# Performance work log

Hardware: AMD Instinct MI355X
Metric: run time of the kernel (lower is better)

## Reference

```python
import jax, jax.numpy as jnp
import numpy as np

B, S, D, H = 4, 2048, 1024, 16
DK = D // H


def setup_inputs() -> dict:
    key = jax.random.key(0)
    ks = jax.random.split(key, 12)
    std = 1.0 / np.sqrt(D)
    return {
        "query": jax.random.normal(ks[0], (B, S, D), jnp.float32),
        "key": jax.random.normal(ks[1], (B, S, D), jnp.float32),
        "value": jax.random.normal(ks[2], (B, S, D), jnp.float32),
        "fc_w": jax.random.normal(ks[3], (D, D), jnp.float32),
        "Wq": jax.random.normal(ks[4], (D, D), jnp.float32) * std,
        "bq": jax.random.normal(ks[5], (D,), jnp.float32) * 0.01,
        "Wk": jax.random.normal(ks[6], (D, D), jnp.float32) * std,
        "bk": jax.random.normal(ks[7], (D,), jnp.float32) * 0.01,
        "Wv": jax.random.normal(ks[8], (D, D), jnp.float32) * std,
        "bv": jax.random.normal(ks[9], (D,), jnp.float32) * 0.01,
        "Wo": jax.random.normal(ks[10], (D, D), jnp.float32) * std,
        "bo": jax.random.normal(ks[11], (D,), jnp.float32) * 0.01,
    }


def reference(query, key, value, fc_w, Wq, bq, Wk, bk, Wv, bv, Wo, bo):
    b = query.shape[0]
    # meta-modulated (scaling) query projection: x @ (fc_w * base_w) + b
    q = jnp.matmul(query, fc_w * Wq) + bq
    k = jnp.matmul(key, Wk) + bk
    v = jnp.matmul(value, Wv) + bv
    # [B, S, D] -> [B, H, S, DK]
    q = q.reshape(b, -1, H, DK).transpose(0, 2, 1, 3)
    k = k.reshape(b, -1, H, DK).transpose(0, 2, 1, 3)
    v = v.reshape(b, -1, H, DK).transpose(0, 2, 1, 3)
    scores = jnp.einsum("bhqd,bhkd->bhqk", q, k) / jnp.sqrt(jnp.float32(DK))
    attn = jax.nn.softmax(scores, axis=-1)  # dropout identity at eval
    x = jnp.einsum("bhqk,bhkd->bhqd", attn, v)
    x = x.transpose(0, 2, 1, 3).reshape(b, -1, H * DK)
    return jnp.matmul(x, Wo) + bo
```

## Files before the change

### kernel.cpp

```cpp
#include <hip/hip_runtime.h>
#include <hip/hip_bf16.h>
#include <stdint.h>

#define BB 4
#define SS 2048
#define DD 1024
#define HH 16
#define DKK 64
#define MT (BB*SS)
#define KK DD

typedef __attribute__((ext_vector_type(8))) short bf16x8;
typedef __attribute__((ext_vector_type(4))) float f32x4;
typedef __attribute__((ext_vector_type(8))) unsigned short u16x8;

__device__ __forceinline__ unsigned short f2bf(float f){
  union { float f; unsigned u; } x; x.f = f;
  unsigned r = x.u + 0x7fffu + ((x.u >> 16) & 1u);
  return (unsigned short)(r >> 16);
}

__device__ __forceinline__ short bfc(float x){
  return (short)__builtin_bit_cast(unsigned short, (__bf16)x);
}

__device__ __forceinline__ float ex2(float x){
#if __has_builtin(__builtin_amdgcn_exp2f)
  return __builtin_amdgcn_exp2f(x);
#else
  return exp2f(x);
#endif
}

__device__ __forceinline__ float fm3(float a, float b, float c){
  return fmaxf(fmaxf(a, b), c);
}

__device__ __forceinline__ void gll16(const void* g, void* l){
  __builtin_amdgcn_global_load_lds(
      (const __attribute__((address_space(1))) void*)g,
      (__attribute__((address_space(3))) void*)l, 16, 0, 0);
}

__global__ __launch_bounds__(256) void cvt_bf16(const float* __restrict__ in,
                                                unsigned short* __restrict__ out){
  int i = blockIdx.x * 256 + threadIdx.x;
  const f32x4* p = (const f32x4*)in;
  f32x4 a = p[2*i], b = p[2*i+1];
  u16x8 o;
  #pragma unroll
  for (int j=0;j<4;j++){ o[j] = f2bf(a[j]); o[4+j] = f2bf(b[j]); }
  ((u16x8*)out)[i] = o;
}

__global__ __launch_bounds__(256) void prep_weights(
    const float* __restrict__ fc, const float* __restrict__ Wq,
    const float* __restrict__ Wk, const float* __restrict__ Wv,
    const float* __restrict__ Wo,
    unsigned short* __restrict__ Wqt, unsigned short* __restrict__ Wkt,
    unsigned short* __restrict__ Wvt, unsigned short* __restrict__ Wot){
  __shared__ float tile[32][33];
  int which = blockIdx.y;
  const float* src = which==0?Wq: which==1?Wk: which==2?Wv:Wo;
  unsigned short* dst = which==0?Wqt: which==1?Wkt: which==2?Wvt:Wot;
  int k0 = (blockIdx.x & 31)*32, n0 = (blockIdx.x >> 5)*32;
  int tid = threadIdx.x;
  #pragma unroll
  for (int i=0;i<4;i++){
    int e = tid + i*256; int r = e>>5, c = e&31;
    float v = src[(size_t)(k0+r)*DD + n0 + c];
    if (which==0) v *= fc[(size_t)(k0+r)*DD + n0 + c];
    tile[r][c] = v;
  }
  __syncthreads();
  #pragma unroll
  for (int i=0;i<4;i++){
    int e = tid + i*256; int r = e>>5, c = e&31;
    dst[(size_t)(n0+r)*DD + k0 + c] = f2bf(tile[c][r]);
  }
}

template<int EPI>
__global__ __launch_bounds__(256) void gemm_bt(
    const unsigned short* __restrict__ A,
    const unsigned short* __restrict__ Bt,
    const float* __restrict__ bias,
    float scale,
    void* __restrict__ Cout){
  __shared__ __align__(16) unsigned short Asb[2][128*32];
  __shared__ __align__(16) unsigned short Bsb[2][128*32];
  const int tid = threadIdx.x;
  const int lane = tid & 63, wid = tid >> 6;
  const int sidx = blockIdx.x;
  const int xcd = sidx & 7, jj = sidx >> 3;
  const int by = xcd*8 + (jj>>3), bx = jj & 7;
  const int m0 = by * 128, n0 = bx * 128;
  const int wm = wid >> 1, wn = wid & 1;
  const int g = lane >> 4, lr = lane & 15;

  f32x4 acc[4][4];
  #pragma unroll
  for (int i=0;i<4;i++)
    #pragma unroll
    for (int j=0;j<4;j++) acc[i][j] = (f32x4){0.f,0.f,0.f,0.f};

  const char* gaBase = (const char*)(A  + (size_t)m0 * KK);
  const char* gbBase = (const char*)(Bt + (size_t)n0 * KK);

  auto stage = [&](int buf, int kt){
    #pragma unroll
    for (int is=0; is<2; ++is){
      int t = is*4096 + wid*1024 + lane*16;
      int row = t >> 6, col = t & 63;
      gll16(gaBase + (size_t)row*(KK*2) + (size_t)kt*64 + col,
            (char*)&Asb[buf][0] + is*4096 + wid*1024);
      gll16(gbBase + (size_t)row*(KK*2) + (size_t)kt*64 + col,
            (char*)&Bsb[buf][0] + is*4096 + wid*1024);
    }
  };

  stage(0, 0);
  __syncthreads();
  int cur = 0;
  for (int kt = 0; kt < KK/32; ++kt){
    if (kt + 1 < KK/32) stage(cur^1, kt+1);
    bf16x8 af[4], bfr[4];
    #pragma unroll
    for (int f=0; f<4; ++f){
      int ar = wm*64 + f*16 + lr;
      af[f]  = *(const bf16x8*)&Asb[cur][ar*32 + g*8];
      int br = wn*64 + f*16 + lr;
      bfr[f] = *(const bf16x8*)&Bsb[cur][br*32 + g*8];
    }
    #pragma unroll
    for (int i=0;i<4;i++)
      #pragma unroll
      for (int j=0;j<4;j++)
        acc[i][j] = __builtin_amdgcn_mfma_f32_16x16x32_bf16(af[i], bfr[j], acc[i][j], 0, 0, 0);
    __syncthreads();
    cur ^= 1;
  }

  #pragma unroll
  for (int j=0;j<4;j++){
    int n = n0 + wn*64 + j*16 + lr;
    float bv = bias[n];
    #pragma unroll
    for (int i=0;i<4;i++){
      int mbase = m0 + wm*64 + i*16 + g*4;
      #pragma unroll
      for (int r=0;r<4;r++){
        int m = mbase + r;
        float v = (acc[i][j][r] + bv) * scale;
        if (EPI == 0){
          int b = m >> 11, s = m & (SS-1);
          int h = n >> 6, dk = n & 63;
          ((unsigned short*)Cout)[(((size_t)(b*HH + h))*SS + s)*DKK + dk] = f2bf(v);
        } else {
          ((float*)Cout)[(size_t)m*DD + n] = v;
        }
      }
    }
  }
}

__global__ __launch_bounds__(256) void transpose_v(const unsigned short* __restrict__ V,
                                                   unsigned short* __restrict__ Vt){
  __shared__ unsigned short t[64][72];
  int bh = blockIdx.y; int s0 = blockIdx.x*64;
  const unsigned short* src = V + ((size_t)bh*SS + s0)*DKK;
  int tid = threadIdx.x;
  #pragma unroll
  for (int i=0;i<2;i++){
    int e = (tid + i*256)*8; int r = e>>6, c = e&63;
    int rp = (r & 35) | ((r & 12) << 1) | ((r & 16) >> 2);
    u16x8 v = *(const u16x8*)(src + (size_t)r*DKK + c);
    #pragma unroll
    for (int j=0;j<8;j++) t[c+j][rp] = v[j];
  }
  __syncthreads();
  unsigned short* dst = Vt + ((size_t)bh*DKK)*SS + s0;
  #pragma unroll
  for (int i=0;i<2;i++){
    int e = (tid + i*256)*8; int d = e>>6, c = e&63;
    u16x8 v = *(const u16x8*)(&t[d][c]);
    *(u16x8*)(dst + (size_t)d*SS + c) = v;
  }
}

__global__ __launch_bounds__(256) void attn(
    const unsigned short* __restrict__ Qg,
    const unsigned short* __restrict__ Kg,
    const unsigned short* __restrict__ Vtg,
    unsigned short* __restrict__ Xg){
  __shared__ __align__(16) unsigned short Qs[64*64];
  __shared__ __align__(16) unsigned short Ks[2][64*64];
  __shared__ __align__(16) unsigned short Vs[2][64*64];
  const int tid = threadIdx.x;
  const int lane = tid & 63, wid = tid >> 6;
  const int g = lane >> 4, lr = lane & 15;
  const int bh = blockIdx.y;
  const int q0 = blockIdx.x * 64;

  const char* Qbase = (const char*)(Qg + ((size_t)bh*SS + q0)*DKK);
  const char* Kbase = (const char*)(Kg + (size_t)bh*SS*DKK);
  const char* Vbase = (const char*)(Vtg + (size_t)bh*DKK*SS);

  #pragma unroll
  for (int is=0; is<2; ++is){
    int t = is*4096 + wid*1024 + lane*16;
    int row = t >> 7;
    int col = (t & 127) ^ ((row & 7) << 4);
    gll16(Qbase + row*128 + col, (char*)Qs + is*4096 + wid*1024);
  }

  auto stageK = [&](int buf, int it){
    const char* gk = Kbase + (size_t)it*8192;
    #pragma unroll
    for (int is=0; is<2; ++is){
      int t = is*4096 + wid*1024 + lane*16;
      int row = t >> 7;
      int col = (t & 127) ^ ((row & 7) << 4);
      gll16(gk + row*128 + col, (char*)&Ks[buf][0] + is*4096 + wid*1024);
    }
  };
  auto stageV = [&](int buf, int it){
    #pragma unroll
    for (int is=0; is<2; ++is){
      int t = is*4096 + wid*1024 + lane*16;
      int row = t >> 7;
      int col = (t & 127) ^ ((row & 7) << 4);
      gll16(Vbase + (size_t)row*(SS*2) + (size_t)it*128 + col,
            (char*)&Vs[buf][0] + is*4096 + wid*1024);
    }
  };

  stageK(0, 0); stageV(0, 0);
  __syncthreads();

  bf16x8 qf[2];
  {
    int qrow = wid*16 + lr;
    int sw = (qrow & 7) << 4;
    #pragma unroll
    for (int h2=0; h2<2; ++h2){
      int cb = (g*8 + h2*32) * 2;
      qf[h2] = *(const bf16x8*)((const char*)Qs + qrow*128 + (cb ^ sw));
    }
  }

  f32x4 Xf[4];
  #pragma unroll
  for (int d=0; d<4; ++d) Xf[d] = (f32x4){0.f,0.f,0.f,0.f};
  const f32x4 Zv = (f32x4){0.f,0.f,0.f,0.f};
  float m2 = -1e30f, ell = 0.f;

  const int sw2 = (lr & 7) << 4;

  auto body = [&](int cb){
    const char* Kb = (const char*)&Ks[cb][0];
    const char* Vb = (const char*)&Vs[cb][0];
    f32x4 st[4];
    __builtin_amdgcn_s_setprio(1);
    #pragma unroll
    for (int s4=0; s4<4; ++s4){
      int rb = (s4*16 + lr) * 128;
      bf16x8 k0 = *(const bf16x8*)(Kb + rb + ((g*16     ) ^ sw2));
      bf16x8 k1 = *(const bf16x8*)(Kb + rb + ((g*16 + 64) ^ sw2));
      st[s4] = __builtin_amdgcn_mfma_f32_16x16x32_bf16(k0, qf[0], Zv,     0,0,0);
      st[s4] = __builtin_amdgcn_mfma_f32_16x16x32_bf16(k1, qf[1], st[s4], 0,0,0);
    }
    __builtin_amdgcn_s_setprio(0);

    float t0 = fm3(st[0][0], st[0][1], st[0][2]);
    float t1 = fm3(st[0][3], st[1][0], st[1][1]);
    float t2 = fm3(st[1][2], st[1][3], st[2][0]);
    float t3 = fm3(st[2][1], st[2][2], st[2][3]);
    float t4 = fm3(st[3][0], st[3][1], st[3][2]);
    float tmax = fm3(fm3(t0, t1, t2), fmaxf(t3, t4), st[3][3]);
    tmax = fmaxf(tmax, __shfl_xor(tmax, 16));
    tmax = fmaxf(tmax, __shfl_xor(tmax, 32));
    if (__any(tmax > m2 + 8.f)){
      float mn = fmaxf(m2, tmax);
      float sc = ex2(m2 - mn);
      m2 = mn;
      ell *= sc;
      #pragma unroll
      for (int r=0; r<4; ++r){
        float scr = __shfl(sc, g*4 + r);
        #pragma unroll
        for (int d=0; d<4; ++d) Xf[d][r] *= scr;
      }
    }
    float p[4][4];
    #pragma unroll
    for (int s4=0; s4<4; ++s4)
      #pragma unroll
      for (int r=0; r<4; ++r) p[s4][r] = ex2(st[s4][r] - m2);
    float ps0 = (p[0][0]+p[0][1]) + (p[0][2]+p[0][3]);
    float ps1 = (p[1][0]+p[1][1]) + (p[1][2]+p[1][3]);
    float ps2 = (p[2][0]+p[2][1]) + (p[2][2]+p[2][3]);
    float ps3 = (p[3][0]+p[3][1]) + (p[3][2]+p[3][3]);
    ell += (ps0+ps1) + (ps2+ps3);

    bf16x8 pa0, pa1;
    #pragma unroll
    for (int j=0; j<8; ++j){
      pa0[j] = bfc(p[(j>>2)    ][j&3]);
      pa1[j] = bfc(p[2 + (j>>2)][j&3]);
    }

    __builtin_amdgcn_s_setprio(1);
    #pragma unroll
    for (int d=0; d<4; ++d){
      int rb = (d*16 + lr) * 128;
      bf16x8 b0 = *(const bf16x8*)(Vb + rb + ((g*16     ) ^ sw2));
      bf16x8 b1 = *(const bf16x8*)(Vb + rb + ((g*16 + 64) ^ sw2));
      Xf[d] = __builtin_amdgcn_mfma_f32_16x16x32_bf16(pa0, b0, Xf[d], 0,0,0);
      Xf[d] = __builtin_amdgcn_mfma_f32_16x16x32_bf16(pa1, b1, Xf[d], 0,0,0);
    }
    __builtin_amdgcn_s_setprio(0);
  };

  for (int it = 0; it < SS/64; it += 2){
    if (it + 1 < SS/64){ stageK(1, it+1); stageV(1, it+1); }
    body(0);
    __syncthreads();
    if (it + 2 < SS/64){ stageK(0, it+2); stageV(0, it+2); }
    body(1);
    __syncthreads();
  }

  float elt = ell;
  elt += __shfl_xor(elt, 16);
  elt += __shfl_xor(elt, 32);
  float rinv[4];
  #pragma unroll
  for (int r=0; r<4; ++r) rinv[r] = 1.0f / __shfl(elt, g*4 + r);
  int b = bh >> 4, h = bh & 15;
  #pragma unroll
  for (int d=0; d<4; ++d)
    #pragma unroll
    for (int r=0; r<4; ++r){
      int s = q0 + wid*16 + g*4 + r;
      int col = h*64 + d*16 + lr;
      Xg[((size_t)b*SS + s)*DD + col] = f2bf(Xf[d][r] * rinv[r]);
    }
}

extern "C" void kernel_launch(void* const* d_in, const int* in_sizes, int n_in,
                              void* d_out, int out_size, void* d_ws, size_t ws_size,
                              hipStream_t stream){
  (void)in_sizes; (void)n_in; (void)out_size; (void)ws_size;
  const float* query = (const float*)d_in[0];
  const float* key   = (const float*)d_in[1];
  const float* value = (const float*)d_in[2];
  const float* fc_w  = (const float*)d_in[3];
  const float* Wq    = (const float*)d_in[4];
  const float* bq    = (const float*)d_in[5];
  const float* Wk    = (const float*)d_in[6];
  const float* bk    = (const float*)d_in[7];
  const float* Wv    = (const float*)d_in[8];
  const float* bv    = (const float*)d_in[9];
  const float* Wo    = (const float*)d_in[10];
  const float* bo    = (const float*)d_in[11];

  char* ws = (char*)d_ws;
  const size_t EL = (size_t)BB*SS*DD;
  size_t off = 0;
  auto alloc = [&](size_t bytes){ size_t o = off; off += (bytes + 255) & ~(size_t)255; return o; };
  unsigned short* qb  = (unsigned short*)(ws + alloc(EL*2));
  unsigned short* kb  = (unsigned short*)(ws + alloc(EL*2));
  unsigned short* vb  = (unsigned short*)(ws + alloc(EL*2));
  unsigned short* Wqt = (unsigned short*)(ws + alloc((size_t)DD*DD*2));
  unsigned short* Wkt = (unsigned short*)(ws + alloc((size_t)DD*DD*2));
  unsigned short* Wvt = (unsigned short*)(ws + alloc((size_t)DD*DD*2));
  unsigned short* Wot = (unsigned short*)(ws + alloc((size_t)DD*DD*2));
  unsigned short* Qh  = (unsigned short*)(ws + alloc(EL*2));
  unsigned short* Kh  = (unsigned short*)(ws + alloc(EL*2));
  unsigned short* Vh  = (unsigned short*)(ws + alloc(EL*2));
  unsigned short* Vth = vb;
  unsigned short* Xh  = qb;

  const float SC2 = 0.18033688011112042f;

  const int nbCvt = (int)(EL / 8 / 256);
  cvt_bf16<<<nbCvt, 256, 0, stream>>>(query, qb);
  cvt_bf16<<<nbCvt, 256, 0, stream>>>(key,   kb);
  cvt_bf16<<<nbCvt, 256, 0, stream>>>(value, vb);
  prep_weights<<<dim3(1024, 4), 256, 0, stream>>>(fc_w, Wq, Wk, Wv, Wo, Wqt, Wkt, Wvt, Wot);

  gemm_bt<0><<<512, 256, 0, stream>>>(qb, Wqt, bq, SC2, Qh);
  gemm_bt<0><<<512, 256, 0, stream>>>(kb, Wkt, bk, 1.0f, Kh);
  gemm_bt<0><<<512, 256, 0, stream>>>(vb, Wvt, bv, 1.0f, Vh);

  transpose_v<<<dim3(SS/64, BB*HH), 256, 0, stream>>>(Vh, Vth);
  attn<<<dim3(SS/64, BB*HH), 256, 0, stream>>>(Qh, Kh, Vth, Xh);

  gemm_bt<1><<<512, 256, 0, stream>>>(Xh, Wot, bo, 1.0f, d_out);
}
```

Baseline: 402.1 us.

## Batch QKV GEMMs into one launch and double query rows per attention wave

The three Q/K/V projection GEMMs are merged into a single 1536-block launch that picks operands from the block index, which cuts launch overhead and fills the GPU better. The attention kernel now gives each wave two 16-row query tiles (128 queries per block), so every K/V tile staged in LDS is reused across twice as many queries. Query fragments are loaded straight from global memory instead of through LDS. The cost is more registers per thread (two accumulator and softmax state sets) and half as many attention blocks, which may lower occupancy.

```diff
diff --git a/kernel.cpp b/kernel.cpp
--- a/kernel.cpp
+++ b/kernel.cpp
@@ -80,88 +80,108 @@
   }
 }
 
-template<int EPI>
-__global__ __launch_bounds__(256) void gemm_bt(
-    const unsigned short* __restrict__ A,
-    const unsigned short* __restrict__ Bt,
-    const float* __restrict__ bias,
-    float scale,
-    void* __restrict__ Cout){
+#define GEMM_BODY(EPI, A, Bt, bias, scale, Cout, m0, n0)                          \
+  {                                                                               \
+  const int tid = threadIdx.x;                                                    \
+  const int lane = tid & 63, wid = tid >> 6;                                      \
+  const int wm = wid >> 1, wn = wid & 1;                                          \
+  const int g = lane >> 4, lr = lane & 15;                                        \
+  f32x4 acc[4][4];                                                                \
+  _Pragma("unroll")                                                               \
+  for (int i=0;i<4;i++)                                                           \
+    _Pragma("unroll")                                                             \
+    for (int j=0;j<4;j++) acc[i][j] = (f32x4){0.f,0.f,0.f,0.f};                   \
+  const char* gaBase = (const char*)((A)  + (size_t)(m0) * KK);                   \
+  const char* gbBase = (const char*)((Bt) + (size_t)(n0) * KK);                   \
+  auto stage = [&](int buf, int kt){                                              \
+    _Pragma("unroll")                                                             \
+    for (int is=0; is<2; ++is){                                                   \
+      int t = is*4096 + wid*1024 + lane*16;                                       \
+      int row = t >> 6, col = t & 63;                                             \
+      gll16(gaBase + (size_t)row*(KK*2) + (size_t)kt*64 + col,                    \
+            (char*)&Asb[buf][0] + is*4096 + wid*1024);                            \
+      gll16(gbBase + (size_t)row*(KK*2) + (size_t)kt*64 + col,                    \
+            (char*)&Bsb[buf][0] + is*4096 + wid*1024);                            \
+    }                                                                             \
+  };                                                                              \
+  stage(0, 0);                                                                    \
+  __syncthreads();                                                                \
+  int cur = 0;                                                                    \
+  for (int kt = 0; kt < KK/32; ++kt){                                             \
+    if (kt + 1 < KK/32) stage(cur^1, kt+1);                                       \
+    bf16x8 af[4], bfr[4];                                                         \
+    _Pragma("unroll")                                                             \
+    for (int f=0; f<4; ++f){                                                      \
+      int ar = wm*64 + f*16 + lr;                                                 \
+      af[f]  = *(const bf16x8*)&Asb[cur][ar*32 + g*8];                            \
+      int br = wn*64 + f*16 + lr;                                                 \
+      bfr[f] = *(const bf16x8*)&Bsb[cur][br*32 + g*8];                            \
+    }                                                                             \
+    _Pragma("unroll")                                                             \
+    for (int i=0;i<4;i++)                                                         \
+      _Pragma("unroll")                                                           \
+      for (int j=0;j<4;j++)                                                       \
+        acc[i][j] = __builtin_amdgcn_mfma_f32_16x16x32_bf16(af[i], bfr[j], acc[i][j], 0, 0, 0); \
+    __syncthreads();                                                              \
+    cur ^= 1;                                                                     \
+  }                                                                               \
+  _Pragma("unroll")                                                               \
+  for (int j=0;j<4;j++){                                                          \
+    int n = (n0) + wn*64 + j*16 + lr;                                             \
+    float bv = (bias)[n];                                                         \
+    _Pragma("unroll")                                                             \
+    for (int i=0;i<4;i++){                                                        \
+      int mbase = (m0) + wm*64 + i*16 + g*4;                                      \
+      _Pragma("unroll")                                                           \
+      for (int r=0;r<4;r++){                                                      \
+        int m = mbase + r;                                                        \
+        float v = (acc[i][j][r] + bv) * (scale);                                  \
+        if (EPI == 0){                                                            \
+          int b = m >> 11, s = m & (SS-1);                                        \
+          int h = n >> 6, dk = n & 63;                                            \
+          ((unsigned short*)(Cout))[(((size_t)(b*HH + h))*SS + s)*DKK + dk] = f2bf(v); \
+        } else {                                                                  \
+          ((float*)(Cout))[(size_t)m*DD + n] = v;                                 \
+        }                                                                         \
+      }                                                                           \
+    }                                                                             \
+  }                                                                               \
+  }
+
+__global__ __launch_bounds__(256) void gemm_qkv(
+    const unsigned short* __restrict__ Aq, const unsigned short* __restrict__ Ak,
+    const unsigned short* __restrict__ Av,
+    const unsigned short* __restrict__ Wq, const unsigned short* __restrict__ Wk,
+    const unsigned short* __restrict__ Wv,
+    const float* __restrict__ bq, const float* __restrict__ bk,
+    const float* __restrict__ bv, float qscale,
+    unsigned short* __restrict__ Qo, unsigned short* __restrict__ Ko,
+    unsigned short* __restrict__ Vo){
   __shared__ __align__(16) unsigned short Asb[2][128*32];
   __shared__ __align__(16) unsigned short Bsb[2][128*32];
-  const int tid = threadIdx.x;
-  const int lane = tid & 63, wid = tid >> 6;
+  const int u = blockIdx.x;
+  const int which = u % 3, v = u / 3;
+  const int xcd = v & 7, jj = v >> 3;
+  const int by = xcd*8 + (jj>>3), bx = jj & 7;
+  const int m0 = by * 128, n0 = bx * 128;
+  const unsigned short* A  = which==0 ? Aq : which==1 ? Ak : Av;
+  const unsigned short* Bt = which==0 ? Wq : which==1 ? Wk : Wv;
+  const float* bias        = which==0 ? bq : which==1 ? bk : bv;
+  unsigned short* C        = which==0 ? Qo : which==1 ? Ko : Vo;
+  float scale = which==0 ? qscale : 1.0f;
+  GEMM_BODY(0, A, Bt, bias, scale, C, m0, n0)
+}
+
+__global__ __launch_bounds__(256) void gemm_o(
+    const unsigned short* __restrict__ A, const unsigned short* __restrict__ Bt,
+    const float* __restrict__ bias, float* __restrict__ Cout){
+  __shared__ __align__(16) unsigned short Asb[2][128*32];
+  __shared__ __align__(16) unsigned short Bsb[2][128*32];
   const int sidx = blockIdx.x;
   const int xcd = sidx & 7, jj = sidx >> 3;
   const int by = xcd*8 + (jj>>3), bx = jj & 7;
   const int m0 = by * 128, n0 = bx * 128;
-  const int wm = wid >> 1, wn = wid & 1;
-  const int g = lane >> 4, lr = lane & 15;
-
-  f32x4 acc[4][4];
-  #pragma unroll
-  for (int i=0;i<4;i++)
-    #pragma unroll
-    for (int j=0;j<4;j++) acc[i][j] = (f32x4){0.f,0.f,0.f,0.f};
-
-  const char* gaBase = (const char*)(A  + (size_t)m0 * KK);
-  const char* gbBase = (const char*)(Bt + (size_t)n0 * KK);
-
-  auto stage = [&](int buf, int kt){
-    #pragma unroll
-    for (int is=0; is<2; ++is){
-      int t = is*4096 + wid*1024 + lane*16;
-      int row = t >> 6, col = t & 63;
-      gll16(gaBase + (size_t)row*(KK*2) + (size_t)kt*64 + col,
-            (char*)&Asb[buf][0] + is*4096 + wid*1024);
-      gll16(gbBase + (size_t)row*(KK*2) + (size_t)kt*64 + col,
-            (char*)&Bsb[buf][0] + is*4096 + wid*1024);
-    }
-  };
-
-  stage(0, 0);
-  __syncthreads();
-  int cur = 0;
-  for (int kt = 0; kt < KK/32; ++kt){
-    if (kt + 1 < KK/32) stage(cur^1, kt+1);
-    bf16x8 af[4], bfr[4];
-    #pragma unroll
-    for (int f=0; f<4; ++f){
-      int ar = wm*64 + f*16 + lr;
-      af[f]  = *(const bf16x8*)&Asb[cur][ar*32 + g*8];
-      int br = wn*64 + f*16 + lr;
-      bfr[f] = *(const bf16x8*)&Bsb[cur][br*32 + g*8];
-    }
-    #pragma unroll
-    for (int i=0;i<4;i++)
-      #pragma unroll
-      for (int j=0;j<4;j++)
-        acc[i][j] = __builtin_amdgcn_mfma_f32_16x16x32_bf16(af[i], bfr[j], acc[i][j], 0, 0, 0);
-    __syncthreads();
-    cur ^= 1;
-  }
-
-  #pragma unroll
-  for (int j=0;j<4;j++){
-    int n = n0 + wn*64 + j*16 + lr;
-    float bv = bias[n];
-    #pragma unroll
-    for (int i=0;i<4;i++){
-      int mbase = m0 + wm*64 + i*16 + g*4;
-      #pragma unroll
-      for (int r=0;r<4;r++){
-        int m = mbase + r;
-        float v = (acc[i][j][r] + bv) * scale;
-        if (EPI == 0){
-          int b = m >> 11, s = m & (SS-1);
-          int h = n >> 6, dk = n & 63;
-          ((unsigned short*)Cout)[(((size_t)(b*HH + h))*SS + s)*DKK + dk] = f2bf(v);
-        } else {
-          ((float*)Cout)[(size_t)m*DD + n] = v;
-        }
-      }
-    }
-  }
+  GEMM_BODY(1, A, Bt, bias, 1.0f, Cout, m0, n0)
 }
 
 __global__ __launch_bounds__(256) void transpose_v(const unsigned short* __restrict__ V,
@@ -193,26 +213,17 @@
     const unsigned short* __restrict__ Kg,
     const unsigned short* __restrict__ Vtg,
     unsigned short* __restrict__ Xg){
-  __shared__ __align__(16) unsigned short Qs[64*64];
   __shared__ __align__(16) unsigned short Ks[2][64*64];
   __shared__ __align__(16) unsigned short Vs[2][64*64];
   const int tid = threadIdx.x;
   const int lane = tid & 63, wid = tid >> 6;
   const int g = lane >> 4, lr = lane & 15;
   const int bh = blockIdx.y;
-  const int q0 = blockIdx.x * 64;
-
-  const char* Qbase = (const char*)(Qg + ((size_t)bh*SS + q0)*DKK);
+  const int q0 = blockIdx.x * 128;
+
+  const unsigned short* Qrow = Qg + ((size_t)bh*SS + q0)*DKK;
   const char* Kbase = (const char*)(Kg + (size_t)bh*SS*DKK);
   const char* Vbase = (const char*)(Vtg + (size_t)bh*DKK*SS);
-
-  #pragma unroll
-  for (int is=0; is<2; ++is){
-    int t = is*4096 + wid*1024 + lane*16;
-    int row = t >> 7;
-    int col = (t & 127) ^ ((row & 7) << 4);
-    gll16(Qbase + row*128 + col, (char*)Qs + is*4096 + wid*1024);
-  }
 
   auto stageK = [&](int buf, int it){
     const char* gk = Kbase + (size_t)it*8192;
@@ -236,78 +247,81 @@
   };
 
   stageK(0, 0); stageV(0, 0);
+
+  bf16x8 qf[2][2];
+  #pragma unroll
+  for (int u=0; u<2; ++u){
+    int qrow = wid*32 + u*16 + lr;
+    #pragma unroll
+    for (int h2=0; h2<2; ++h2)
+      qf[u][h2] = *(const bf16x8*)(Qrow + (size_t)qrow*DKK + g*8 + h2*32);
+  }
+
+  f32x4 Xf[2][4];
+  #pragma unroll
+  for (int u=0; u<2; ++u)
+    #pragma unroll
+    for (int d=0; d<4; ++d) Xf[u][d] = (f32x4){0.f,0.f,0.f,0.f};
+  const f32x4 Zv = (f32x4){0.f,0.f,0.f,0.f};
+  float m2[2] = {-1e30f, -1e30f}, ell[2] = {0.f, 0.f};
+  const int sw2 = (lr & 7) << 4;
+
   __syncthreads();
 
-  bf16x8 qf[2];
-  {
-    int qrow = wid*16 + lr;
-    int sw = (qrow & 7) << 4;
-    #pragma unroll
-    for (int h2=0; h2<2; ++h2){
-      int cb = (g*8 + h2*32) * 2;
-      qf[h2] = *(const bf16x8*)((const char*)Qs + qrow*128 + (cb ^ sw));
-    }
-  }
-
-  f32x4 Xf[4];
-  #pragma unroll
-  for (int d=0; d<4; ++d) Xf[d] = (f32x4){0.f,0.f,0.f,0.f};
-  const f32x4 Zv = (f32x4){0.f,0.f,0.f,0.f};
-  float m2 = -1e30f, ell = 0.f;
-
-  const int sw2 = (lr & 7) << 4;
-
-  auto body = [&](int cb){
-    const char* Kb = (const char*)&Ks[cb][0];
-    const char* Vb = (const char*)&Vs[cb][0];
-    f32x4 st[4];
+  auto body = [&](int cbuf){
+    const char* Kb = (const char*)&Ks[cbuf][0];
+    const char* Vb = (const char*)&Vs[cbuf][0];
+    f32x4 st[4][2];
     __builtin_amdgcn_s_setprio(1);
     #pragma unroll
     for (int s4=0; s4<4; ++s4){
       int rb = (s4*16 + lr) * 128;
       bf16x8 k0 = *(const bf16x8*)(Kb + rb + ((g*16     ) ^ sw2));
       bf16x8 k1 = *(const bf16x8*)(Kb + rb + ((g*16 + 64) ^ sw2));
-      st[s4] = __builtin_amdgcn_mfma_f32_16x16x32_bf16(k0, qf[0], Zv,     0,0,0);
-      st[s4] = __builtin_amdgcn_mfma_f32_16x16x32_bf16(k1, qf[1], st[s4], 0,0,0);
+      st[s4][0] = __builtin_amdgcn_mfma_f32_16x16x32_bf16(k0, qf[0][0], Zv,        0,0,0);
+      st[s4][0] = __builtin_amdgcn_mfma_f32_16x16x32_bf16(k1, qf[0][1], st[s4][0], 0,0,0);
+      st[s4][1] = __builtin_amdgcn_mfma_f32_16x16x32_bf16(k0, qf[1][0], Zv,        0,0,0);
+      st[s4][1] = __builtin_amdgcn_mfma_f32_16x16x32_bf16(k1, qf[1][1], st[s4][1], 0,0,0);
     }
     __builtin_amdgcn_s_setprio(0);
 
-    float t0 = fm3(st[0][0], st[0][1], st[0][2]);
-    float t1 = fm3(st[0][3], st[1][0], st[1][1]);
-    float t2 = fm3(st[1][2], st[1][3], st[2][0]);
-    float t3 = fm3(st[2][1], st[2][2], st[2][3]);
-    float t4 = fm3(st[3][0], st[3][1], st[3][2]);
-    float tmax = fm3(fm3(t0, t1, t2), fmaxf(t3, t4), st[3][3]);
-    tmax = fmaxf(tmax, __shfl_xor(tmax, 16));
-    tmax = fmaxf(tmax, __shfl_xor(tmax, 32));
-    if (__any(tmax > m2 + 8.f)){
-      float mn = fmaxf(m2, tmax);
-      float sc = ex2(m2 - mn);
-      m2 = mn;
-      ell *= sc;
+    bf16x8 pa[2][2];
+    #pragma unroll
+    for (int u=0; u<2; ++u){
+      float t0 = fm3(st[0][u][0], st[0][u][1], st[0][u][2]);
+      float t1 = fm3(st[0][u][3], st[1][u][0], st[1][u][1]);
+      float t2 = fm3(st[1][u][2], st[1][u][3], st[2][u][0]);
+      float t3 = fm3(st[2][u][1], st[2][u][2], st[2][u][3]);
+      float t4 = fm3(st[3][u][0], st[3][u][1], st[3][u][2]);
+      float tmax = fm3(fm3(t0, t1, t2), fmaxf(t3, t4), st[3][u][3]);
+      tmax = fmaxf(tmax, __shfl_xor(tmax, 16));
+      tmax = fmaxf(tmax, __shfl_xor(tmax, 32));
+      if (__any(tmax > m2[u] + 8.f)){
+        float mn = fmaxf(m2[u], tmax);
+        float sc = ex2(m2[u] - mn);
+        m2[u] = mn;
+        ell[u] *= sc;
+        #pragma unroll
+        for (int r=0; r<4; ++r){
+          float scr = __shfl(sc, g*4 + r);
+          #pragma unroll
+          for (int d=0; d<4; ++d) Xf[u][d][r] *= scr;
+        }
+      }
       #pragma unroll
-      for (int r=0; r<4; ++r){
-        float scr = __shfl(sc, g*4 + r);
+      for (int s4=0; s4<4; ++s4)
         #pragma unroll
-        for (int d=0; d<4; ++d) Xf[d][r] *= scr;
+        for (int r=0; r<4; ++r) st[s4][u][r] = ex2(st[s4][u][r] - m2[u]);
+      float ps0 = (st[0][u][0]+st[0][u][1]) + (st[0][u][2]+st[0][u][3]);
+      float ps1 = (st[1][u][0]+st[1][u][1]) + (st[1][u][2]+st[1][u][3]);
+      float ps2 = (st[2][u][0]+st[2][u][1]) + (st[2][u][2]+st[2][u][3]);
+      float ps3 = (st[3][u][0]+st[3][u][1]) + (st[3][u][2]+st[3][u][3]);
+      ell[u] += (ps0+ps1) + (ps2+ps3);
+      #pragma unroll
+      for (int j=0; j<8; ++j){
+        pa[u][0][j] = bfc(st[(j>>2)    ][u][j&3]);
+        pa[u][1][j] = bfc(st[2 + (j>>2)][u][j&3]);
       }
-    }
-    float p[4][4];
-    #pragma unroll
-    for (int s4=0; s4<4; ++s4)
-      #pragma unroll
-      for (int r=0; r<4; ++r) p[s4][r] = ex2(st[s4][r] - m2);
-    float ps0 = (p[0][0]+p[0][1]) + (p[0][2]+p[0][3]);
-    float ps1 = (p[1][0]+p[1][1]) + (p[1][2]+p[1][3]);
-    float ps2 = (p[2][0]+p[2][1]) + (p[2][2]+p[2][3]);
-    float ps3 = (p[3][0]+p[3][1]) + (p[3][2]+p[3][3]);
-    ell += (ps0+ps1) + (ps2+ps3);
-
-    bf16x8 pa0, pa1;
-    #pragma unroll
-    for (int j=0; j<8; ++j){
-      pa0[j] = bfc(p[(j>>2)    ][j&3]);
-      pa1[j] = bfc(p[2 + (j>>2)][j&3]);
     }
 
     __builtin_amdgcn_s_setprio(1);
@@ -316,8 +330,10 @@
       int rb = (d*16 + lr) * 128;
       bf16x8 b0 = *(const bf16x8*)(Vb + rb + ((g*16     ) ^ sw2));
       bf16x8 b1 = *(const bf16x8*)(Vb + rb + ((g*16 + 64) ^ sw2));
-      Xf[d] = __builtin_amdgcn_mfma_f32_16x16x32_bf16(pa0, b0, Xf[d], 0,0,0);
-      Xf[d] = __builtin_amdgcn_mfma_f32_16x16x32_bf16(pa1, b1, Xf[d], 0,0,0);
+      Xf[0][d] = __builtin_amdgcn_mfma_f32_16x16x32_bf16(pa[0][0], b0, Xf[0][d], 0,0,0);
+      Xf[0][d] = __builtin_amdgcn_mfma_f32_16x16x32_bf16(pa[0][1], b1, Xf[0][d], 0,0,0);
+      Xf[1][d] = __builtin_amdgcn_mfma_f32_16x16x32_bf16(pa[1][0], b0, Xf[1][d], 0,0,0);
+      Xf[1][d] = __builtin_amdgcn_mfma_f32_16x16x32_bf16(pa[1][1], b1, Xf[1][d], 0,0,0);
     }
     __builtin_amdgcn_s_setprio(0);
   };
@@ -331,21 +347,24 @@
     __syncthreads();
   }
 
-  float elt = ell;
-  elt += __shfl_xor(elt, 16);
-  elt += __shfl_xor(elt, 32);
-  float rinv[4];
-  #pragma unroll
-  for (int r=0; r<4; ++r) rinv[r] = 1.0f / __shfl(elt, g*4 + r);
   int b = bh >> 4, h = bh & 15;
   #pragma unroll
-  for (int d=0; d<4; ++d)
-    #pragma unroll
-    for (int r=0; r<4; ++r){
-      int s = q0 + wid*16 + g*4 + r;
-      int col = h*64 + d*16 + lr;
-      Xg[((size_t)b*SS + s)*DD + col] = f2bf(Xf[d][r] * rinv[r]);
-    }
+  for (int u=0; u<2; ++u){
+    float elt = ell[u];
+    elt += __shfl_xor(elt, 16);
+    elt += __shfl_xor(elt, 32);
+    float rinv[4];
+    #pragma unroll
+    for (int r=0; r<4; ++r) rinv[r] = 1.0f / __shfl(elt, g*4 + r);
+    #pragma unroll
+    for (int d=0; d<4; ++d)
+      #pragma unroll
+      for (int r=0; r<4; ++r){
+        int s = q0 + wid*32 + u*16 + g*4 + r;
+        int col = h*64 + d*16 + lr;
+        Xg[((size_t)b*SS + s)*DD + col] = f2bf(Xf[u][d][r] * rinv[r]);
+      }
+  }
 }
 
 extern "C" void kernel_launch(void* const* d_in, const int* in_sizes, int n_in,
@@ -390,12 +409,11 @@
   cvt_bf16<<<nbCvt, 256, 0, stream>>>(value, vb);
   prep_weights<<<dim3(1024, 4), 256, 0, stream>>>(fc_w, Wq, Wk, Wv, Wo, Wqt, Wkt, Wvt, Wot);
 
-  gemm_bt<0><<<512, 256, 0, stream>>>(qb, Wqt, bq, SC2, Qh);
-  gemm_bt<0><<<512, 256, 0, stream>>>(kb, Wkt, bk, 1.0f, Kh);
-  gemm_bt<0><<<512, 256, 0, stream>>>(vb, Wvt, bv, 1.0f, Vh);
+  gemm_qkv<<<1536, 256, 0, stream>>>(qb, kb, vb, Wqt, Wkt, Wvt, bq, bk, bv, SC2,
+                                     Qh, Kh, Vh);
 
   transpose_v<<<dim3(SS/64, BB*HH), 256, 0, stream>>>(Vh, Vth);
-  attn<<<dim3(SS/64, BB*HH), 256, 0, stream>>>(Qh, Kh, Vth, Xh);
-
-  gemm_bt<1><<<512, 256, 0, stream>>>(Xh, Wot, bo, 1.0f, d_out);
-}
+  attn<<<dim3(SS/128, BB*HH), 256, 0, stream>>>(Qh, Kh, Vth, Xh);
+
+  gemm_o<<<512, 256, 0, stream>>>(Xh, Wot, bo, (float*)d_out);
+}
```

Measured after the change: 379.6 us. 1.06x faster.
